# Optimization experiments

Measured on AMD Instinct MI355X. Metric: run time of the kernel, lower is better.

The kernel has to match this reference:

```python
import jax, jax.numpy as jnp
import numpy as np

BETA = 1.0  # nn.SmoothL1Loss() default; module's self.beta=0.5 is never used


def smooth_l1(d):
    ad = jnp.abs(d)
    return jnp.where(ad < BETA, 0.5 * d * d / BETA, ad - 0.5 * BETA)


def setup_inputs() -> dict:
    key = jax.random.key(0)
    k1, k2, k3 = jax.random.split(key, 3)
    B, T, D = 32, 2048, 512
    preds = jax.random.normal(k1, (B, T, D), dtype=jnp.float32)
    targets = jax.random.normal(k2, (B, T, D), dtype=jnp.float32)
    # lengths in [1, T], sorted descending (pack_padded_sequence convention)
    decode_lengths = jnp.sort(jax.random.randint(k3, (B,), 1, T + 1))[::-1]
    return {"preds": preds, "targets": targets, "decode_lengths": decode_lengths}


def reference(preds, targets, decode_lengths):
    B, T, D = preds.shape
    mask = (jnp.arange(T)[None, :] < decode_lengths[:, None]).astype(preds.dtype)  # [B,T]
    lens = decode_lengths.astype(preds.dtype)[:, None]  # [B,1]

    # sentence loss: SmoothL1 between per-sample time-means, mean over D, summed over B
    pred_mean = jnp.einsum('btd,bt->bd', preds, mask) / lens
    targ_mean = jnp.einsum('btd,bt->bd', targets, mask) / lens
    sentence_loss = jnp.sum(jnp.mean(smooth_l1(pred_mean - targ_mean), axis=1))

    # word loss: SmoothL1 over all valid (packed) elements, mean reduction
    elem = smooth_l1(preds - targets) * mask[:, :, None]
    n_valid = jnp.sum(decode_lengths).astype(preds.dtype) * D
    word_loss = jnp.sum(elem) / n_valid

    return word_loss + sentence_loss / B
```

## Files before the change

kernel.cpp:

```cpp
#include <hip/hip_runtime.h>


#define BATCH 32
#define TLEN  2048
#define DDIM  512
#define ROWS_PER_BLOCK 32
#define P1_THREADS 128

__device__ __forceinline__ float sl1(float d) {
    float ad = fabsf(d);
    return ad < 1.0f ? 0.5f * d * d : ad - 0.5f;
}

__global__ __launch_bounds__(P1_THREADS)
void pass1(const float* __restrict__ preds, const float* __restrict__ targs,
           const int* __restrict__ lens,
           float* __restrict__ colp, float* __restrict__ colt,
           float* __restrict__ wacc)
{
    const int b     = blockIdx.x;
    const int chunk = blockIdx.y;
    const int len   = lens[b];
    const int t0    = chunk * ROWS_PER_BLOCK;
    if (t0 >= len) return;
    const int t1 = min(t0 + ROWS_PER_BLOCK, len);

    const float4* __restrict__ p4 =
        (const float4*)(preds + (size_t)b * TLEN * DDIM);
    const float4* __restrict__ q4 =
        (const float4*)(targs + (size_t)b * TLEN * DDIM);
    const int lane4 = threadIdx.x;

    float4 sp = make_float4(0.f, 0.f, 0.f, 0.f);
    float4 st = make_float4(0.f, 0.f, 0.f, 0.f);
    float  w  = 0.f;

    for (int t = t0; t < t1; ++t) {
        float4 p = p4[(size_t)t * (DDIM / 4) + lane4];
        float4 q = q4[(size_t)t * (DDIM / 4) + lane4];
        sp.x += p.x; sp.y += p.y; sp.z += p.z; sp.w += p.w;
        st.x += q.x; st.y += q.y; st.z += q.z; st.w += q.w;
        w += sl1(p.x - q.x) + sl1(p.y - q.y) + sl1(p.z - q.z) + sl1(p.w - q.w);
    }

    float* cp = colp + b * DDIM + lane4 * 4;
    float* ct = colt + b * DDIM + lane4 * 4;
    atomicAdd(cp + 0, sp.x); atomicAdd(cp + 1, sp.y);
    atomicAdd(cp + 2, sp.z); atomicAdd(cp + 3, sp.w);
    atomicAdd(ct + 0, st.x); atomicAdd(ct + 1, st.y);
    atomicAdd(ct + 2, st.z); atomicAdd(ct + 3, st.w);

    #pragma unroll
    for (int off = 32; off; off >>= 1) w += __shfl_down(w, off);
    __shared__ float ws[P1_THREADS / 64];
    if ((threadIdx.x & 63) == 0) ws[threadIdx.x >> 6] = w;
    __syncthreads();
    if (threadIdx.x == 0) {
        float tot = 0.f;
        #pragma unroll
        for (int i = 0; i < P1_THREADS / 64; ++i) tot += ws[i];
        atomicAdd(wacc, tot);
    }
}

__global__ __launch_bounds__(1024)
void pass2(const float* __restrict__ colp, const float* __restrict__ colt,
           const int* __restrict__ lens, const float* __restrict__ wacc,
           float* __restrict__ out)
{
    const int tid = threadIdx.x;
    float s = 0.f;
    for (int i = tid; i < BATCH * DDIM; i += 1024) {
        const int b = i >> 9;
        const float L = (float)lens[b];
        const float d = (colp[i] - colt[i]) / L;
        s += sl1(d);
    }
    #pragma unroll
    for (int off = 32; off; off >>= 1) s += __shfl_down(s, off);
    __shared__ float red[16];
    if ((tid & 63) == 0) red[tid >> 6] = s;
    __syncthreads();
    if (tid == 0) {
        float sent = 0.f;
        #pragma unroll
        for (int i = 0; i < 16; ++i) sent += red[i];
        float nvalid = 0.f;
        for (int b = 0; b < BATCH; ++b) nvalid += (float)lens[b];
        const float word_loss = wacc[0] / (nvalid * (float)DDIM);
        const float sent_loss = sent / ((float)DDIM * (float)BATCH);
        out[0] = word_loss + sent_loss;
    }
}

extern "C" void kernel_launch(void* const* d_in, const int* in_sizes, int n_in,
                              void* d_out, int out_size, void* d_ws, size_t ws_size,
                              hipStream_t stream) {
    const float* preds = (const float*)d_in[0];
    const float* targs = (const float*)d_in[1];
    const int*   lens  = (const int*)d_in[2];
    float* out = (float*)d_out;

    float* colp = (float*)d_ws;
    float* colt = colp + BATCH * DDIM;
    float* wacc = colt + BATCH * DDIM;
    const size_t ws_bytes = (size_t)(2 * BATCH * DDIM + 1) * sizeof(float);
    hipMemsetAsync(d_ws, 0, ws_bytes, stream);

    dim3 grid1(BATCH, TLEN / ROWS_PER_BLOCK);
    pass1<<<grid1, P1_THREADS, 0, stream>>>(preds, targs, lens, colp, colt, wacc);
    pass2<<<1, 1024, 0, stream>>>(colp, colt, lens, wacc, out);
}
```

Baseline: 268.4 us.

## Replace atomic column accumulation with per-chunk partials and a staged reduction

```diff
diff --git a/kernel.cpp b/kernel.cpp
--- a/kernel.cpp
+++ b/kernel.cpp
@@ -4,7 +4,8 @@
 #define BATCH 32
 #define TLEN  2048
 #define DDIM  512
-#define ROWS_PER_BLOCK 32
+#define CHUNK 16
+#define NCH   (TLEN / CHUNK)
 #define P1_THREADS 128
 
 __device__ __forceinline__ float sl1(float d) {
@@ -15,40 +16,49 @@
 __global__ __launch_bounds__(P1_THREADS)
 void pass1(const float* __restrict__ preds, const float* __restrict__ targs,
            const int* __restrict__ lens,
-           float* __restrict__ colp, float* __restrict__ colt,
-           float* __restrict__ wacc)
+           float4* __restrict__ colp_part,
+           float4* __restrict__ colt_part,
+           float* __restrict__ wpart)
 {
-    const int b     = blockIdx.x;
-    const int chunk = blockIdx.y;
-    const int len   = lens[b];
-    const int t0    = chunk * ROWS_PER_BLOCK;
+    const int b   = blockIdx.x;
+    const int c   = blockIdx.y;
+    const int len = lens[b];
+    const int t0  = c * CHUNK;
     if (t0 >= len) return;
-    const int t1 = min(t0 + ROWS_PER_BLOCK, len);
+    const int t1  = min(t0 + CHUNK, len);
 
-    const float4* __restrict__ p4 =
-        (const float4*)(preds + (size_t)b * TLEN * DDIM);
-    const float4* __restrict__ q4 =
-        (const float4*)(targs + (size_t)b * TLEN * DDIM);
+    const float4* __restrict__ p4 = (const float4*)(preds + (size_t)b * TLEN * DDIM);
+    const float4* __restrict__ q4 = (const float4*)(targs + (size_t)b * TLEN * DDIM);
     const int lane4 = threadIdx.x;
 
     float4 sp = make_float4(0.f, 0.f, 0.f, 0.f);
     float4 st = make_float4(0.f, 0.f, 0.f, 0.f);
     float  w  = 0.f;
 
-    for (int t = t0; t < t1; ++t) {
-        float4 p = p4[(size_t)t * (DDIM / 4) + lane4];
-        float4 q = q4[(size_t)t * (DDIM / 4) + lane4];
-        sp.x += p.x; sp.y += p.y; sp.z += p.z; sp.w += p.w;
-        st.x += q.x; st.y += q.y; st.z += q.z; st.w += q.w;
-        w += sl1(p.x - q.x) + sl1(p.y - q.y) + sl1(p.z - q.z) + sl1(p.w - q.w);
+    if (t1 - t0 == CHUNK) {
+        #pragma unroll
+        for (int i = 0; i < CHUNK; ++i) {
+            const size_t r = (size_t)(t0 + i) * (DDIM / 4) + lane4;
+            float4 p = p4[r];
+            float4 q = q4[r];
+            sp.x += p.x; sp.y += p.y; sp.z += p.z; sp.w += p.w;
+            st.x += q.x; st.y += q.y; st.z += q.z; st.w += q.w;
+            w += sl1(p.x - q.x) + sl1(p.y - q.y) + sl1(p.z - q.z) + sl1(p.w - q.w);
+        }
+    } else {
+        for (int t = t0; t < t1; ++t) {
+            const size_t r = (size_t)t * (DDIM / 4) + lane4;
+            float4 p = p4[r];
+            float4 q = q4[r];
+            sp.x += p.x; sp.y += p.y; sp.z += p.z; sp.w += p.w;
+            st.x += q.x; st.y += q.y; st.z += q.z; st.w += q.w;
+            w += sl1(p.x - q.x) + sl1(p.y - q.y) + sl1(p.z - q.z) + sl1(p.w - q.w);
+        }
     }
 
-    float* cp = colp + b * DDIM + lane4 * 4;
-    float* ct = colt + b * DDIM + lane4 * 4;
-    atomicAdd(cp + 0, sp.x); atomicAdd(cp + 1, sp.y);
-    atomicAdd(cp + 2, sp.z); atomicAdd(cp + 3, sp.w);
-    atomicAdd(ct + 0, st.x); atomicAdd(ct + 1, st.y);
-    atomicAdd(ct + 2, st.z); atomicAdd(ct + 3, st.w);
+    const size_t slot = (size_t)(b * NCH + c) * (DDIM / 4) + lane4;
+    colp_part[slot] = sp;
+    colt_part[slot] = st;
 
     #pragma unroll
     for (int off = 32; off; off >>= 1) w += __shfl_down(w, off);
@@ -59,36 +69,70 @@
         float tot = 0.f;
         #pragma unroll
         for (int i = 0; i < P1_THREADS / 64; ++i) tot += ws[i];
-        atomicAdd(wacc, tot);
+        wpart[b * NCH + c] = tot;
     }
 }
 
-__global__ __launch_bounds__(1024)
-void pass2(const float* __restrict__ colp, const float* __restrict__ colt,
-           const int* __restrict__ lens, const float* __restrict__ wacc,
-           float* __restrict__ out)
+__global__ __launch_bounds__(P1_THREADS)
+void pass2(const float4* __restrict__ colp_part, const float4* __restrict__ colt_part,
+           const float* __restrict__ wpart, const int* __restrict__ lens,
+           float* __restrict__ sentb,
+           float* __restrict__ wordb)
 {
-    const int tid = threadIdx.x;
-    float s = 0.f;
-    for (int i = tid; i < BATCH * DDIM; i += 1024) {
-        const int b = i >> 9;
-        const float L = (float)lens[b];
-        const float d = (colp[i] - colt[i]) / L;
-        s += sl1(d);
+    const int b   = blockIdx.x;
+    const int len = lens[b];
+    const int nch = (len + CHUNK - 1) / CHUNK;
+    const int t   = threadIdx.x;
+
+    float4 sp = make_float4(0.f, 0.f, 0.f, 0.f);
+    float4 st = make_float4(0.f, 0.f, 0.f, 0.f);
+    for (int c = 0; c < nch; ++c) {
+        const size_t slot = (size_t)(b * NCH + c) * (DDIM / 4) + t;
+        float4 p = colp_part[slot];
+        float4 q = colt_part[slot];
+        sp.x += p.x; sp.y += p.y; sp.z += p.z; sp.w += p.w;
+        st.x += q.x; st.y += q.y; st.z += q.z; st.w += q.w;
     }
+    const float invL = 1.0f / (float)len;
+    float s = sl1((sp.x - st.x) * invL) + sl1((sp.y - st.y) * invL)
+            + sl1((sp.z - st.z) * invL) + sl1((sp.w - st.w) * invL);
+
+    float wsum = 0.f;
+    for (int c = t; c < nch; c += P1_THREADS) wsum += wpart[b * NCH + c];
+
     #pragma unroll
-    for (int off = 32; off; off >>= 1) s += __shfl_down(s, off);
-    __shared__ float red[16];
-    if ((tid & 63) == 0) red[tid >> 6] = s;
+    for (int off = 32; off; off >>= 1) {
+        s    += __shfl_down(s, off);
+        wsum += __shfl_down(wsum, off);
+    }
+    __shared__ float rs[P1_THREADS / 64], rw[P1_THREADS / 64];
+    if ((t & 63) == 0) { rs[t >> 6] = s; rw[t >> 6] = wsum; }
     __syncthreads();
-    if (tid == 0) {
-        float sent = 0.f;
+    if (t == 0) {
+        float st_ = 0.f, wt_ = 0.f;
         #pragma unroll
-        for (int i = 0; i < 16; ++i) sent += red[i];
-        float nvalid = 0.f;
-        for (int b = 0; b < BATCH; ++b) nvalid += (float)lens[b];
-        const float word_loss = wacc[0] / (nvalid * (float)DDIM);
-        const float sent_loss = sent / ((float)DDIM * (float)BATCH);
+        for (int i = 0; i < P1_THREADS / 64; ++i) { st_ += rs[i]; wt_ += rw[i]; }
+        sentb[b] = st_;
+        wordb[b] = wt_;
+    }
+}
+
+__global__ __launch_bounds__(64)
+void pass3(const float* __restrict__ sentb, const float* __restrict__ wordb,
+           const int* __restrict__ lens, float* __restrict__ out)
+{
+    const int t = threadIdx.x;
+    float s = 0.f, w = 0.f, L = 0.f;
+    if (t < BATCH) { s = sentb[t]; w = wordb[t]; L = (float)lens[t]; }
+    #pragma unroll
+    for (int off = 32; off; off >>= 1) {
+        s += __shfl_down(s, off);
+        w += __shfl_down(w, off);
+        L += __shfl_down(L, off);
+    }
+    if (t == 0) {
+        const float word_loss = w / (L * (float)DDIM);
+        const float sent_loss = s / ((float)DDIM * (float)BATCH);
         out[0] = word_loss + sent_loss;
     }
 }
@@ -102,12 +146,15 @@
     float* out = (float*)d_out;
 
     float* colp = (float*)d_ws;
-    float* colt = colp + BATCH * DDIM;
-    float* wacc = colt + BATCH * DDIM;
-    const size_t ws_bytes = (size_t)(2 * BATCH * DDIM + 1) * sizeof(float);
-    hipMemsetAsync(d_ws, 0, ws_bytes, stream);
+    float* colt = colp + (size_t)BATCH * NCH * DDIM;
+    float* wpart = colt + (size_t)BATCH * NCH * DDIM;
+    float* sentb = wpart + BATCH * NCH;
+    float* wordb = sentb + BATCH;
 
-    dim3 grid1(BATCH, TLEN / ROWS_PER_BLOCK);
-    pass1<<<grid1, P1_THREADS, 0, stream>>>(preds, targs, lens, colp, colt, wacc);
-    pass2<<<1, 1024, 0, stream>>>(colp, colt, lens, wacc, out);
+    dim3 grid1(BATCH, NCH);
+    pass1<<<grid1, P1_THREADS, 0, stream>>>(preds, targs, lens,
+                                            (float4*)colp, (float4*)colt, wpart);
+    pass2<<<BATCH, P1_THREADS, 0, stream>>>((const float4*)colp, (const float4*)colt,
+                                            wpart, lens, sentb, wordb);
+    pass3<<<1, 64, 0, stream>>>(sentb, wordb, lens, out);
 }
```

Result: slower. 285.3 us (+6.3%).
